# Performance work log

Measured on AMD Instinct MI355X. Metric: run time of the kernel, lower is better.

Reference implementation:

```python
import jax, jax.numpy as jnp
import numpy as np

B, H, W, C = 2, 96, 96, 96
GROUPS = 32
EPS = 1e-5


def group_norm_dim1(x, gamma, beta):
    # Faithful to torch nn.GroupNorm(32, C) applied to an NHWC tensor:
    # dim 1 (H) is treated as the channel axis, normalized over (H//G, W, C) per group.
    b, h, w, c = x.shape
    xg = x.reshape(b, GROUPS, h // GROUPS, w, c)
    mean = xg.mean(axis=(2, 3, 4), keepdims=True)
    var = xg.var(axis=(2, 3, 4), keepdims=True)
    xn = ((xg - mean) * jax.lax.rsqrt(var + EPS)).reshape(b, h, w, c)
    return xn * gamma[None, :, None, None] + beta[None, :, None, None]


def setup_inputs() -> dict:
    key = jax.random.key(0)
    ks = jax.random.split(key, 9)
    s = 1.0 / np.sqrt(C)  # kaiming-uniform-ish scale
    x = jax.random.normal(ks[0], (B, H, W, C), dtype=jnp.float32)
    Wq = jax.random.uniform(ks[1], (C, C), jnp.float32, -s, s)
    Wk = jax.random.uniform(ks[2], (C, C), jnp.float32, -s, s)
    Wv = jax.random.uniform(ks[3], (C, C), jnp.float32, -s, s)
    Wp = jax.random.uniform(ks[4], (C, C), jnp.float32, -s, s)
    return {
        "x": x,
        "gamma": jnp.ones((H,), jnp.float32),   # GroupNorm affine weight (over dim 1)
        "beta": jnp.zeros((H,), jnp.float32),
        "Wq": Wq, "bq": jnp.zeros((C,), jnp.float32),
        "Wk": Wk, "bk": jnp.zeros((C,), jnp.float32),
        "Wv": Wv, "bv": jnp.zeros((C,), jnp.float32),
        "Wp": Wp, "bp": jnp.zeros((C,), jnp.float32),
    }


def reference(x, gamma, beta, Wq, bq, Wk, bk, Wv, bv, Wp, bp):
    b, h, w, c = x.shape
    hn = group_norm_dim1(x, gamma, beta)
    q = hn @ Wq + bq  # [B,H,W,C], Nin = contract last dim
    k = hn @ Wk + bk
    v = hn @ Wv + bv
    scale = c ** (-0.5)
    # full dense spatial attention: [B, HW, HW]
    scores = jnp.einsum('bxyc,buvc->bxyuv', q, k) * scale
    attn = jax.nn.softmax(scores.reshape(b, h, w, h * w), axis=-1).reshape(b, h, w, h, w)
    o = jnp.einsum('bxyuv,buvc->bxyc', attn, v)
    return x + (o @ Wp + bp)
```

## Files before the change

kernel.cpp:

```cpp
#include <hip/hip_runtime.h>
#include <hip/hip_bf16.h>
#include <stdint.h>

#define B_   2
#define H_   96
#define W_   96
#define C_   96
#define HW_  (H_ * W_)
#define NT_  (B_ * HW_)
#define EPS_ 1e-5f
#define KSPLIT  8
#define KRANGE  (HW_ / KSPLIT)
#define ATT_NIT (KRANGE / 32)
#define SCL (0.10206207261596575f * 1.4426950408889634f)

typedef __hip_bfloat16 bf16;
typedef __attribute__((ext_vector_type(8))) short short8;
typedef __attribute__((ext_vector_type(16))) float f32x16;

__device__ __forceinline__ uint32_t pk_bf16(float a, float b) {
    uint32_t ua = __float_as_uint(a) + 0x8000u;
    uint32_t ub = __float_as_uint(b) + 0x8000u;
    return __builtin_amdgcn_perm(ub, ua, 0x07060302u);
}
__device__ __forceinline__ float bl(uint32_t u) { uint32_t x = u << 16;         return *(float*)&x; }
__device__ __forceinline__ float bh(uint32_t u) { uint32_t x = u & 0xffff0000u; return *(float*)&x; }
__device__ __forceinline__ float fexp2(float x) { return __builtin_amdgcn_exp2f(x); }
__device__ __forceinline__ short8 lds_frag(const short* p) {
    union { int2 h[2]; short8 v; } t;
    t.h[0] = *(const int2*)(p);
    t.h[1] = *(const int2*)(p + 4);
    return t.v;
}

__device__ __forceinline__ void load_hn_frags(
        const float* __restrict__ x, const float2* __restrict__ stats,
        const float* __restrict__ gamma, const float* __restrict__ beta,
        int token, int hh, short8* hf) {
    int b = token / HW_;
    int h = (token % HW_) / W_;
    float2 st = stats[b * 32 + h / 3];
    float g0 = gamma[h];
    float ga = g0 * st.y;
    float be = beta[h] - st.x * st.y * g0;
    const float* xr = x + (size_t)token * C_ + hh * 8;
    #pragma unroll
    for (int s = 0; s < 6; ++s) {
        float4 a = *(const float4*)(xr + s * 16);
        float4 c = *(const float4*)(xr + s * 16 + 4);
        union { uint32_t w[4]; short8 v; } f;
        f.w[0] = pk_bf16(a.x * ga + be, a.y * ga + be);
        f.w[1] = pk_bf16(a.z * ga + be, a.w * ga + be);
        f.w[2] = pk_bf16(c.x * ga + be, c.y * ga + be);
        f.w[3] = pk_bf16(c.z * ga + be, c.w * ga + be);
        hf[s] = f.v;
    }
}

__global__ __launch_bounds__(1024)
void stats_prep_kernel(const float* __restrict__ x, float2* __restrict__ stats,
                       const float* __restrict__ Wq, const float* __restrict__ Wk,
                       const float* __restrict__ Wv, const float* __restrict__ Wp,
                       bf16* __restrict__ wqt, bf16* __restrict__ wkt,
                       bf16* __restrict__ wvt, bf16* __restrict__ wpt) {
    int blk = blockIdx.x;
    int tid = threadIdx.x;
    if (blk >= 64) {
        int wsel = blk - 64;
        const float* S = (wsel == 0) ? Wq : (wsel == 1) ? Wk : (wsel == 2) ? Wv : Wp;
        bf16* D = (wsel == 0) ? wqt : (wsel == 1) ? wkt : (wsel == 2) ? wvt : wpt;
        for (int i = tid; i < C_ * C_; i += 1024) {
            int r = i / C_, c = i % C_;
            D[c * C_ + r] = __float2bfloat16(S[r * C_ + c]);
        }
        return;
    }
    int b = blk >> 5, g = blk & 31;
    const int n4 = 3 * W_ * C_ / 4;
    const float4* xb = (const float4*)(x + (size_t)(b * H_ + 3 * g) * (W_ * C_));
    float s = 0.f, ss = 0.f;
    for (int i = tid; i < n4; i += 1024) {
        float4 v = xb[i];
        s  += v.x + v.y + v.z + v.w;
        ss += v.x * v.x + v.y * v.y + v.z * v.z + v.w * v.w;
    }
    #pragma unroll
    for (int off = 1; off < 64; off <<= 1) {
        s  += __shfl_xor(s, off, 64);
        ss += __shfl_xor(ss, off, 64);
    }
    __shared__ float rs[16], rss[16];
    int wid = tid >> 6;
    if ((tid & 63) == 0) { rs[wid] = s; rss[wid] = ss; }
    __syncthreads();
    if (tid == 0) {
        float ts = 0.f, tss = 0.f;
        #pragma unroll
        for (int i = 0; i < 16; ++i) { ts += rs[i]; tss += rss[i]; }
        const float n = 3 * W_ * C_;
        float mean = ts / n;
        float var  = tss / n - mean * mean;
        stats[blk] = make_float2(mean, rsqrtf(var + EPS_));
    }
}

__global__ __launch_bounds__(64)
void qkv_kernel(const float* __restrict__ x, const float2* __restrict__ stats,
                const float* __restrict__ gamma, const float* __restrict__ beta,
                const bf16* __restrict__ wqt, const bf16* __restrict__ wkt,
                const bf16* __restrict__ wvt,
                const float* __restrict__ bq, const float* __restrict__ bk,
                const float* __restrict__ bv,
                bf16* __restrict__ qb, bf16* __restrict__ kb, bf16* __restrict__ vt) {
    int blk = blockIdx.x;
    int w = blk / 576, tile = blk % 576;
    int n0 = tile * 32;
    int lane = threadIdx.x;
    int col = lane & 31, hh = lane >> 5;
    int token = n0 + col;

    short8 hf[6];
    load_hn_frags(x, stats, gamma, beta, token, hh, hf);

    if (w == 2) {
        int bb = n0 / HW_, nl0 = n0 % HW_;
        #pragma unroll
        for (int t = 0; t < 3; ++t) {
            int c = t * 32 + col;
            const bf16* wrow = wvt + (size_t)c * C_ + hh * 8;
            f32x16 acc = (f32x16)(0.f);
            #pragma unroll
            for (int s = 0; s < 6; ++s)
                acc = __builtin_amdgcn_mfma_f32_32x32x16_bf16(
                        hf[s], *(const short8*)(wrow + s * 16), acc, 0, 0, 0);
            float bias = bv[c];
            bf16* dst = vt + ((size_t)bb * C_ + c) * HW_ + nl0 + 4 * hh;
            #pragma unroll
            for (int g = 0; g < 4; ++g) {
                uint2 pk = make_uint2(pk_bf16(acc[4 * g] + bias, acc[4 * g + 1] + bias),
                                      pk_bf16(acc[4 * g + 2] + bias, acc[4 * g + 3] + bias));
                *(uint2*)(dst + 8 * g) = pk;
            }
        }
    } else {
        const bf16*  wt   = (w == 0) ? wqt : wkt;
        const float* bias = (w == 0) ? bq : bk;
        bf16*        dst  = (w == 0) ? qb : kb;
        float        scl  = (w == 0) ? SCL : 1.f;
        #pragma unroll
        for (int t = 0; t < 3; ++t) {
            const bf16* wrow = wt + (size_t)(t * 32 + col) * C_ + hh * 8;
            f32x16 acc = (f32x16)(0.f);
            #pragma unroll
            for (int s = 0; s < 6; ++s)
                acc = __builtin_amdgcn_mfma_f32_32x32x16_bf16(
                        *(const short8*)(wrow + s * 16), hf[s], acc, 0, 0, 0);
            #pragma unroll
            for (int g = 0; g < 4; ++g) {
                int nb = t * 32 + 8 * g + 4 * hh;
                float4 b4 = *(const float4*)(bias + nb);
                float v0 = (acc[4 * g]     + b4.x) * scl;
                float v1 = (acc[4 * g + 1] + b4.y) * scl;
                float v2 = (acc[4 * g + 2] + b4.z) * scl;
                float v3 = (acc[4 * g + 3] + b4.w) * scl;
                uint2 pk = make_uint2(pk_bf16(v0, v1), pk_bf16(v2, v3));
                *(uint2*)(dst + (size_t)token * C_ + nb) = pk;
            }
        }
    }
}

__global__ __launch_bounds__(256, 4)
void attn_kernel(const bf16* __restrict__ qb, const bf16* __restrict__ kb,
                 const bf16* __restrict__ vt,
                 bf16* __restrict__ pob, float* __restrict__ pl) {
    __shared__ short Kbuf[2][32 * 100];
    __shared__ short Vbuf[2][96 * 36];

    int blk = blockIdx.x;
    int ks = blk & 7, qg = blk >> 3;
    int b = qg / 72, g72 = qg % 72;
    int n0 = g72 * 128;
    int tid = threadIdx.x;
    int wave = tid >> 6, lane = tid & 63;
    int col = lane & 31, hh = lane >> 5;

    const bf16* kbb = kb + ((size_t)b * HW_ + (size_t)ks * KRANGE) * C_;
    const bf16* vbb = vt + (size_t)b * C_ * HW_ + (size_t)ks * KRANGE;

    int n = n0 + wave * 32 + col;
    short8 qf[6];
    {
        const bf16* qrow = qb + (size_t)(b * HW_ + n) * C_ + hh * 8;
        #pragma unroll
        for (int s = 0; s < 6; ++s) qf[s] = *(const short8*)(qrow + s * 16);
    }

    f32x16 oa[3];
    #pragma unroll
    for (int t = 0; t < 3; ++t) oa[t] = (f32x16)(0.f);
    float l_run = 0.f;

    bool isK = (tid < 128);
    int t128 = tid & 127;
    int ldsA[3], ldsB[3], goff[3];
    #pragma unroll
    for (int j = 0; j < 3; ++j) {
        int c = t128 + 128 * j;
        if (isK) {
            ldsA[j] = (c / 12) * 100 + (c % 12) * 8;
            ldsB[j] = ldsA[j] + 4;
            goff[j] = c * 8;
        } else {
            int rw = c >> 2, g = c & 3;
            ldsA[j] = rw * 36 + (2 * g - (g & 1)) * 4;
            ldsB[j] = rw * 36 + (2 * g + 2 - (g & 1)) * 4;
            goff[j] = rw * HW_ + g * 8;
        }
    }
    const bf16* gbase = isK ? kbb : vbb;
    const int itstep = isK ? (32 * C_) : 32;

    {
        short* sb = isK ? Kbuf[0] : Vbuf[0];
        #pragma unroll
        for (int j = 0; j < 3; ++j) {
            int4 r = *(const int4*)(gbase + goff[j]);
            *(int2*)(sb + ldsA[j]) = make_int2(r.x, r.y);
            *(int2*)(sb + ldsB[j]) = make_int2(r.z, r.w);
        }
    }
    __syncthreads();

    union FU { uint32_t w[4]; short8 v; };

    for (int it = 0; it < ATT_NIT; ++it) {
        int cur = it & 1;
        bool pre = (it + 1 < ATT_NIT);
        int4 r0, r1, r2;
        if (pre) {
            const bf16* g = gbase + (size_t)(it + 1) * itstep;
            r0 = *(const int4*)(g + goff[0]);
            r1 = *(const int4*)(g + goff[1]);
            r2 = *(const int4*)(g + goff[2]);
        }

        const short* Kc = Kbuf[cur];
        const short* Vc = Vbuf[cur];

        short8 kf[6];
        #pragma unroll
        for (int s = 0; s < 6; ++s)
            kf[s] = lds_frag(Kc + col * 100 + s * 16 + hh * 8);

        f32x16 st = (f32x16)(0.f);
        #pragma unroll
        for (int s = 0; s < 6; ++s)
            st = __builtin_amdgcn_mfma_f32_32x32x16_bf16(kf[s], qf[s], st, 0, 0, 0);

        float p[16], ls = 0.f;
        #pragma unroll
        for (int i = 0; i < 16; ++i) { p[i] = fexp2(st[i]); ls += p[i]; }
        l_run += ls;
        FU f0, f1;
        #pragma unroll
        for (int j = 0; j < 4; ++j) {
            f0.w[j] = pk_bf16(p[2 * j],     p[2 * j + 1]);
            f1.w[j] = pk_bf16(p[8 + 2 * j], p[8 + 2 * j + 1]);
        }

        #pragma unroll
        for (int t = 0; t < 3; ++t) {
            const short* vr = Vc + (32 * t + col) * 36 + hh * 8;
            short8 vf0 = lds_frag(vr);
            short8 vf1 = lds_frag(vr + 16);
            oa[t] = __builtin_amdgcn_mfma_f32_32x32x16_bf16(vf0, f0.v, oa[t], 0, 0, 0);
            oa[t] = __builtin_amdgcn_mfma_f32_32x32x16_bf16(vf1, f1.v, oa[t], 0, 0, 0);
        }

        if (pre) {
            short* sb = isK ? Kbuf[cur ^ 1] : Vbuf[cur ^ 1];
            *(int2*)(sb + ldsA[0]) = make_int2(r0.x, r0.y);
            *(int2*)(sb + ldsB[0]) = make_int2(r0.z, r0.w);
            *(int2*)(sb + ldsA[1]) = make_int2(r1.x, r1.y);
            *(int2*)(sb + ldsB[1]) = make_int2(r1.z, r1.w);
            *(int2*)(sb + ldsA[2]) = make_int2(r2.x, r2.y);
            *(int2*)(sb + ldsB[2]) = make_int2(r2.z, r2.w);
        }
        __syncthreads();
    }

    {
        size_t bq = (size_t)b * HW_ + n;
        float lt = l_run + __shfl_xor(l_run, 32, 64);
        if (hh == 0) pl[(size_t)ks * NT_ + bq] = lt;
        #pragma unroll
        for (int t = 0; t < 3; ++t)
            #pragma unroll
            for (int g = 0; g < 4; ++g) {
                int c0 = t * 32 + 8 * g + 4 * hh;
                uint2 pk = make_uint2(
                    pk_bf16(oa[t][4 * g],     oa[t][4 * g + 1]),
                    pk_bf16(oa[t][4 * g + 2], oa[t][4 * g + 3]));
                *(uint2*)(pob + ((size_t)ks * NT_ + bq) * C_ + c0) = pk;
            }
    }
}

__global__ __launch_bounds__(256)
void out_kernel(const float* __restrict__ x,
                const bf16* __restrict__ pob, const float* __restrict__ pl,
                const bf16* __restrict__ wpt, const float* __restrict__ bp,
                float* __restrict__ out) {
    __shared__ short ofs[32 * 100];
    __shared__ float linv_s[32];

    int tile = blockIdx.x;
    int n0 = tile * 32;
    int tid = threadIdx.x;

    if (tid < 32) {
        int token = n0 + tid;
        float l = 0.f;
        #pragma unroll
        for (int ksp = 0; ksp < KSPLIT; ++ksp) l += pl[(size_t)ksp * NT_ + token];
        linv_s[tid] = 1.f / l;
    }
    __syncthreads();

    for (int pos = tid; pos < 384; pos += 256) {
        int token = pos / 12, c8 = (pos % 12) * 8;
        float acc[8] = {0.f, 0.f, 0.f, 0.f, 0.f, 0.f, 0.f, 0.f};
        #pragma unroll
        for (int ksp = 0; ksp < KSPLIT; ++ksp) {
            uint4 u = *(const uint4*)(pob + ((size_t)ksp * NT_ + n0 + token) * C_ + c8);
            acc[0] += bl(u.x); acc[1] += bh(u.x);
            acc[2] += bl(u.y); acc[3] += bh(u.y);
            acc[4] += bl(u.z); acc[5] += bh(u.z);
            acc[6] += bl(u.w); acc[7] += bh(u.w);
        }
        float inv = linv_s[token];
        short* dst = ofs + token * 100 + c8;
        *(int2*)(dst)     = make_int2(pk_bf16(acc[0] * inv, acc[1] * inv),
                                      pk_bf16(acc[2] * inv, acc[3] * inv));
        *(int2*)(dst + 4) = make_int2(pk_bf16(acc[4] * inv, acc[5] * inv),
                                      pk_bf16(acc[6] * inv, acc[7] * inv));
    }
    __syncthreads();

    int wave = tid >> 6;
    if (wave >= 3) return;
    int lane = tid & 63, col = lane & 31, hh = lane >> 5;
    int t = wave;
    int token = n0 + col;

    short8 of[6];
    #pragma unroll
    for (int s = 0; s < 6; ++s)
        of[s] = lds_frag(ofs + col * 100 + s * 16 + hh * 8);

    f32x16 acc = (f32x16)(0.f);
    const bf16* wrow = wpt + (size_t)(t * 32 + col) * C_ + hh * 8;
    #pragma unroll
    for (int s = 0; s < 6; ++s)
        acc = __builtin_amdgcn_mfma_f32_32x32x16_bf16(
                *(const short8*)(wrow + s * 16), of[s], acc, 0, 0, 0);
    #pragma unroll
    for (int g = 0; g < 4; ++g) {
        int nb = t * 32 + 8 * g + 4 * hh;
        float4 b4 = *(const float4*)(bp + nb);
        float4 xv = *(const float4*)(x + (size_t)token * C_ + nb);
        float4 rr;
        rr.x = xv.x + acc[4 * g]     + b4.x;
        rr.y = xv.y + acc[4 * g + 1] + b4.y;
        rr.z = xv.z + acc[4 * g + 2] + b4.z;
        rr.w = xv.w + acc[4 * g + 3] + b4.w;
        *(float4*)(out + (size_t)token * C_ + nb) = rr;
    }
}

extern "C" void kernel_launch(void* const* d_in, const int* in_sizes, int n_in,
                              void* d_out, int out_size, void* d_ws, size_t ws_size,
                              hipStream_t stream) {
    const float* x     = (const float*)d_in[0];
    const float* gamma = (const float*)d_in[1];
    const float* beta  = (const float*)d_in[2];
    const float* Wq    = (const float*)d_in[3];
    const float* bq    = (const float*)d_in[4];
    const float* Wk    = (const float*)d_in[5];
    const float* bk    = (const float*)d_in[6];
    const float* Wv    = (const float*)d_in[7];
    const float* bv    = (const float*)d_in[8];
    const float* Wp    = (const float*)d_in[9];
    const float* bp    = (const float*)d_in[10];
    float* out = (float*)d_out;

    char* ws = (char*)d_ws;
    const size_t TB = (size_t)NT_ * C_ * 2;
    bf16* qb  = (bf16*)(ws);
    bf16* kb  = (bf16*)(ws + TB);
    bf16* vt  = (bf16*)(ws + 2 * TB);
    bf16* wqt = (bf16*)(ws + 3 * TB);
    bf16* wkt = (bf16*)(ws + 3 * TB + 18432);
    bf16* wvt = (bf16*)(ws + 3 * TB + 2 * 18432);
    bf16* wpt = (bf16*)(ws + 3 * TB + 3 * 18432);
    float2* stats = (float2*)(ws + 3 * TB + 4 * 18432);
    bf16*  pob = (bf16*)(ws + 3 * TB + 4 * 18432 + 512);
    float* pl  = (float*)(ws + 3 * TB + 4 * 18432 + 512
                          + (size_t)KSPLIT * NT_ * C_ * 2);

    hipLaunchKernelGGL(stats_prep_kernel, dim3(68), dim3(1024), 0, stream,
                       x, stats, Wq, Wk, Wv, Wp, wqt, wkt, wvt, wpt);
    hipLaunchKernelGGL(qkv_kernel, dim3(3 * 576), dim3(64), 0, stream,
                       x, stats, gamma, beta, wqt, wkt, wvt, bq, bk, bv, qb, kb, vt);
    hipLaunchKernelGGL(attn_kernel, dim3(1152), dim3(256), 0, stream,
                       qb, kb, vt, pob, pl);
    hipLaunchKernelGGL(out_kernel, dim3(576), dim3(256), 0, stream,
                       x, pob, pl, wpt, bp, out);
}
```

Before: 195.8 us.

## Triple-buffer K/V tiles and software-pipeline QK^T one iteration ahead

```diff
diff --git a/kernel.cpp b/kernel.cpp
--- a/kernel.cpp
+++ b/kernel.cpp
@@ -170,12 +170,12 @@
     }
 }
 
-__global__ __launch_bounds__(256, 4)
+__global__ __launch_bounds__(256, 3)
 void attn_kernel(const bf16* __restrict__ qb, const bf16* __restrict__ kb,
                  const bf16* __restrict__ vt,
                  bf16* __restrict__ pob, float* __restrict__ pl) {
-    __shared__ short Kbuf[2][32 * 100];
-    __shared__ short Vbuf[2][96 * 36];
+    __shared__ short Kbuf[3][32 * 100];
+    __shared__ short Vbuf[3][96 * 36];
 
     int blk = blockIdx.x;
     int ks = blk & 7, qg = blk >> 3;
@@ -222,73 +222,112 @@
     const int itstep = isK ? (32 * C_) : 32;
 
     {
-        short* sb = isK ? Kbuf[0] : Vbuf[0];
+        short* sb0 = isK ? Kbuf[0] : Vbuf[0];
+        short* sb1 = isK ? Kbuf[1] : Vbuf[1];
         #pragma unroll
         for (int j = 0; j < 3; ++j) {
             int4 r = *(const int4*)(gbase + goff[j]);
-            *(int2*)(sb + ldsA[j]) = make_int2(r.x, r.y);
-            *(int2*)(sb + ldsB[j]) = make_int2(r.z, r.w);
+            *(int2*)(sb0 + ldsA[j]) = make_int2(r.x, r.y);
+            *(int2*)(sb0 + ldsB[j]) = make_int2(r.z, r.w);
+        }
+        #pragma unroll
+        for (int j = 0; j < 3; ++j) {
+            int4 r = *(const int4*)(gbase + itstep + goff[j]);
+            *(int2*)(sb1 + ldsA[j]) = make_int2(r.x, r.y);
+            *(int2*)(sb1 + ldsB[j]) = make_int2(r.z, r.w);
         }
     }
     __syncthreads();
 
     union FU { uint32_t w[4]; short8 v; };
 
-    for (int it = 0; it < ATT_NIT; ++it) {
-        int cur = it & 1;
-        bool pre = (it + 1 < ATT_NIT);
-        int4 r0, r1, r2;
-        if (pre) {
-            const bf16* g = gbase + (size_t)(it + 1) * itstep;
-            r0 = *(const int4*)(g + goff[0]);
-            r1 = *(const int4*)(g + goff[1]);
-            r2 = *(const int4*)(g + goff[2]);
-        }
-
-        const short* Kc = Kbuf[cur];
-        const short* Vc = Vbuf[cur];
-
+    f32x16 stA, stB;
+    {
+        const short* Kc = Kbuf[0];
         short8 kf[6];
         #pragma unroll
         for (int s = 0; s < 6; ++s)
             kf[s] = lds_frag(Kc + col * 100 + s * 16 + hh * 8);
-
-        f32x16 st = (f32x16)(0.f);
+        stA = (f32x16)(0.f);
         #pragma unroll
         for (int s = 0; s < 6; ++s)
-            st = __builtin_amdgcn_mfma_f32_32x32x16_bf16(kf[s], qf[s], st, 0, 0, 0);
-
-        float p[16], ls = 0.f;
-        #pragma unroll
-        for (int i = 0; i < 16; ++i) { p[i] = fexp2(st[i]); ls += p[i]; }
-        l_run += ls;
-        FU f0, f1;
-        #pragma unroll
-        for (int j = 0; j < 4; ++j) {
-            f0.w[j] = pk_bf16(p[2 * j],     p[2 * j + 1]);
-            f1.w[j] = pk_bf16(p[8 + 2 * j], p[8 + 2 * j + 1]);
-        }
-
-        #pragma unroll
-        for (int t = 0; t < 3; ++t) {
-            const short* vr = Vc + (32 * t + col) * 36 + hh * 8;
-            short8 vf0 = lds_frag(vr);
-            short8 vf1 = lds_frag(vr + 16);
-            oa[t] = __builtin_amdgcn_mfma_f32_32x32x16_bf16(vf0, f0.v, oa[t], 0, 0, 0);
-            oa[t] = __builtin_amdgcn_mfma_f32_32x32x16_bf16(vf1, f1.v, oa[t], 0, 0, 0);
-        }
-
-        if (pre) {
-            short* sb = isK ? Kbuf[cur ^ 1] : Vbuf[cur ^ 1];
-            *(int2*)(sb + ldsA[0]) = make_int2(r0.x, r0.y);
-            *(int2*)(sb + ldsB[0]) = make_int2(r0.z, r0.w);
-            *(int2*)(sb + ldsA[1]) = make_int2(r1.x, r1.y);
-            *(int2*)(sb + ldsB[1]) = make_int2(r1.z, r1.w);
-            *(int2*)(sb + ldsA[2]) = make_int2(r2.x, r2.y);
-            *(int2*)(sb + ldsB[2]) = make_int2(r2.z, r2.w);
-        }
-        __syncthreads();
-    }
+            stA = __builtin_amdgcn_mfma_f32_32x32x16_bf16(kf[s], qf[s], stA, 0, 0, 0);
+    }
+
+#define ATT_BODY(IT, CUR, NXT, WRT, SC, SN, PRE1, PRE2)                          \
+    {                                                                            \
+        int4 r0, r1, r2;                                                         \
+        if (PRE2) {                                                              \
+            const bf16* g = gbase + (size_t)((IT) + 2) * itstep;                 \
+            r0 = *(const int4*)(g + goff[0]);                                    \
+            r1 = *(const int4*)(g + goff[1]);                                    \
+            r2 = *(const int4*)(g + goff[2]);                                    \
+        }                                                                        \
+        if (PRE1) {                                                              \
+            const short* Kc = Kbuf[NXT];                                         \
+            short8 kf0 = lds_frag(Kc + col * 100 + 0 * 16 + hh * 8);             \
+            short8 kf1 = lds_frag(Kc + col * 100 + 1 * 16 + hh * 8);             \
+            short8 kf2 = lds_frag(Kc + col * 100 + 2 * 16 + hh * 8);             \
+            short8 kf3 = lds_frag(Kc + col * 100 + 3 * 16 + hh * 8);             \
+            short8 kf4 = lds_frag(Kc + col * 100 + 4 * 16 + hh * 8);             \
+            short8 kf5 = lds_frag(Kc + col * 100 + 5 * 16 + hh * 8);             \
+            SN = (f32x16)(0.f);                                                  \
+            SN = __builtin_amdgcn_mfma_f32_32x32x16_bf16(kf0, qf[0], SN, 0, 0, 0); \
+            SN = __builtin_amdgcn_mfma_f32_32x32x16_bf16(kf1, qf[1], SN, 0, 0, 0); \
+            SN = __builtin_amdgcn_mfma_f32_32x32x16_bf16(kf2, qf[2], SN, 0, 0, 0); \
+            SN = __builtin_amdgcn_mfma_f32_32x32x16_bf16(kf3, qf[3], SN, 0, 0, 0); \
+            SN = __builtin_amdgcn_mfma_f32_32x32x16_bf16(kf4, qf[4], SN, 0, 0, 0); \
+            SN = __builtin_amdgcn_mfma_f32_32x32x16_bf16(kf5, qf[5], SN, 0, 0, 0); \
+        }                                                                        \
+        float p[16], ls = 0.f;                                                   \
+        _Pragma("unroll")                                                        \
+        for (int i = 0; i < 16; ++i) { p[i] = fexp2(SC[i]); ls += p[i]; }        \
+        l_run += ls;                                                             \
+        FU f0, f1;                                                               \
+        _Pragma("unroll")                                                        \
+        for (int j = 0; j < 4; ++j) {                                            \
+            f0.w[j] = pk_bf16(p[2 * j],     p[2 * j + 1]);                       \
+            f1.w[j] = pk_bf16(p[8 + 2 * j], p[8 + 2 * j + 1]);                   \
+        }                                                                        \
+        {                                                                        \
+            const short* Vc = Vbuf[CUR];                                         \
+            _Pragma("unroll")                                                    \
+            for (int t = 0; t < 3; ++t) {                                        \
+                const short* vr = Vc + (32 * t + col) * 36 + hh * 8;             \
+                short8 vf0 = lds_frag(vr);                                       \
+                short8 vf1 = lds_frag(vr + 16);                                  \
+                oa[t] = __builtin_amdgcn_mfma_f32_32x32x16_bf16(vf0, f0.v, oa[t], 0, 0, 0); \
+                oa[t] = __builtin_amdgcn_mfma_f32_32x32x16_bf16(vf1, f1.v, oa[t], 0, 0, 0); \
+            }                                                                    \
+        }                                                                        \
+        if (PRE2) {                                                              \
+            short* sb = isK ? Kbuf[WRT] : Vbuf[WRT];                             \
+            *(int2*)(sb + ldsA[0]) = make_int2(r0.x, r0.y);                      \
+            *(int2*)(sb + ldsB[0]) = make_int2(r0.z, r0.w);                      \
+            *(int2*)(sb + ldsA[1]) = make_int2(r1.x, r1.y);                      \
+            *(int2*)(sb + ldsB[1]) = make_int2(r1.z, r1.w);                      \
+            *(int2*)(sb + ldsA[2]) = make_int2(r2.x, r2.y);                      \
+            *(int2*)(sb + ldsB[2]) = make_int2(r2.z, r2.w);                      \
+        }                                                                        \
+        __syncthreads();                                                         \
+    }
+
+    #pragma unroll 1
+    for (int itb = 0; itb < ATT_NIT - 6; itb += 6) {
+        ATT_BODY(itb + 0, 0, 1, 2, stA, stB, 1, 1)
+        ATT_BODY(itb + 1, 1, 2, 0, stB, stA, 1, 1)
+        ATT_BODY(itb + 2, 2, 0, 1, stA, stB, 1, 1)
+        ATT_BODY(itb + 3, 0, 1, 2, stB, stA, 1, 1)
+        ATT_BODY(itb + 4, 1, 2, 0, stA, stB, 1, 1)
+        ATT_BODY(itb + 5, 2, 0, 1, stB, stA, 1, 1)
+    }
+    ATT_BODY(30, 0, 1, 2, stA, stB, 1, 1)
+    ATT_BODY(31, 1, 2, 0, stB, stA, 1, 1)
+    ATT_BODY(32, 2, 0, 1, stA, stB, 1, 1)
+    ATT_BODY(33, 0, 1, 2, stB, stA, 1, 1)
+    ATT_BODY(34, 1, 2, 0, stA, stB, 1, 0)
+    ATT_BODY(35, 2, 0, 1, stB, stA, 0, 0)
+#undef ATT_BODY
 
     {
         size_t bq = (size_t)b * HW_ + n;
```

New measurement: 304.1 us. 1.55x slower.

## Software-pipeline attention loop: overlap PV MMA of previous tile with softmax

Applied to the files above, without the earlier changes.

```diff
diff --git a/kernel.cpp b/kernel.cpp
--- a/kernel.cpp
+++ b/kernel.cpp
@@ -17,6 +17,8 @@
 typedef __hip_bfloat16 bf16;
 typedef __attribute__((ext_vector_type(8))) short short8;
 typedef __attribute__((ext_vector_type(16))) float f32x16;
+
+union FU { uint32_t w[4]; short8 v; };
 
 __device__ __forceinline__ uint32_t pk_bf16(float a, float b) {
     uint32_t ua = __float_as_uint(a) + 0x8000u;
@@ -170,12 +172,83 @@
     }
 }
 
-__global__ __launch_bounds__(256, 4)
+template<int KB, int VPV, int VWR, bool DO_PV, bool PRE>
+__device__ __forceinline__ void att_body(
+        int it,
+        short (&Kbuf)[2][3200], short (&Vbuf)[3][3456],
+        const short8 (&qf)[6], f32x16 (&oa)[3],
+        FU& f0, FU& f1, float& l_run,
+        const bf16* gbase, int goff0, int goff1, int goff2,
+        int ldsA0, int ldsA1, int ldsA2,
+        int ldsB0, int ldsB1, int ldsB2,
+        int itstep, bool isK, int col, int hh) {
+    int4 r0, r1, r2;
+    if (PRE) {
+        const bf16* g = gbase + (size_t)(it + 1) * itstep;
+        r0 = *(const int4*)(g + goff0);
+        r1 = *(const int4*)(g + goff1);
+        r2 = *(const int4*)(g + goff2);
+    }
+    FU p0, p1;
+    p0.v = f0.v; p1.v = f1.v;
+
+    __builtin_amdgcn_s_setprio(1);
+    const short* Kc = Kbuf[KB];
+    short8 kf0 = lds_frag(Kc + col * 100 + 0 * 16 + hh * 8);
+    short8 kf1 = lds_frag(Kc + col * 100 + 1 * 16 + hh * 8);
+    short8 kf2 = lds_frag(Kc + col * 100 + 2 * 16 + hh * 8);
+    short8 kf3 = lds_frag(Kc + col * 100 + 3 * 16 + hh * 8);
+    short8 kf4 = lds_frag(Kc + col * 100 + 4 * 16 + hh * 8);
+    short8 kf5 = lds_frag(Kc + col * 100 + 5 * 16 + hh * 8);
+    f32x16 st = (f32x16)(0.f);
+    st = __builtin_amdgcn_mfma_f32_32x32x16_bf16(kf0, qf[0], st, 0, 0, 0);
+    st = __builtin_amdgcn_mfma_f32_32x32x16_bf16(kf1, qf[1], st, 0, 0, 0);
+    st = __builtin_amdgcn_mfma_f32_32x32x16_bf16(kf2, qf[2], st, 0, 0, 0);
+    st = __builtin_amdgcn_mfma_f32_32x32x16_bf16(kf3, qf[3], st, 0, 0, 0);
+    st = __builtin_amdgcn_mfma_f32_32x32x16_bf16(kf4, qf[4], st, 0, 0, 0);
+    st = __builtin_amdgcn_mfma_f32_32x32x16_bf16(kf5, qf[5], st, 0, 0, 0);
+
+    if (DO_PV) {
+        const short* Vc = Vbuf[VPV];
+        #pragma unroll
+        for (int t = 0; t < 3; ++t) {
+            const short* vr = Vc + (32 * t + col) * 36 + hh * 8;
+            short8 vf0 = lds_frag(vr);
+            short8 vf1 = lds_frag(vr + 16);
+            oa[t] = __builtin_amdgcn_mfma_f32_32x32x16_bf16(vf0, p0.v, oa[t], 0, 0, 0);
+            oa[t] = __builtin_amdgcn_mfma_f32_32x32x16_bf16(vf1, p1.v, oa[t], 0, 0, 0);
+        }
+    }
+
+    float p[16], ls = 0.f;
+    #pragma unroll
+    for (int i = 0; i < 16; ++i) { p[i] = fexp2(st[i]); ls += p[i]; }
+    l_run += ls;
+    #pragma unroll
+    for (int j = 0; j < 4; ++j) {
+        f0.w[j] = pk_bf16(p[2 * j],     p[2 * j + 1]);
+        f1.w[j] = pk_bf16(p[8 + 2 * j], p[8 + 2 * j + 1]);
+    }
+    __builtin_amdgcn_s_setprio(0);
+
+    if (PRE) {
+        short* sb = isK ? (short*)Kbuf[KB ^ 1] : (short*)Vbuf[VWR];
+        *(int2*)(sb + ldsA0) = make_int2(r0.x, r0.y);
+        *(int2*)(sb + ldsB0) = make_int2(r0.z, r0.w);
+        *(int2*)(sb + ldsA1) = make_int2(r1.x, r1.y);
+        *(int2*)(sb + ldsB1) = make_int2(r1.z, r1.w);
+        *(int2*)(sb + ldsA2) = make_int2(r2.x, r2.y);
+        *(int2*)(sb + ldsB2) = make_int2(r2.z, r2.w);
+    }
+    __syncthreads();
+}
+
+__global__ __launch_bounds__(256, 2)
 void attn_kernel(const bf16* __restrict__ qb, const bf16* __restrict__ kb,
                  const bf16* __restrict__ vt,
                  bf16* __restrict__ pob, float* __restrict__ pl) {
     __shared__ short Kbuf[2][32 * 100];
-    __shared__ short Vbuf[2][96 * 36];
+    __shared__ short Vbuf[3][96 * 36];
 
     int blk = blockIdx.x;
     int ks = blk & 7, qg = blk >> 3;
@@ -222,7 +295,7 @@
     const int itstep = isK ? (32 * C_) : 32;
 
     {
-        short* sb = isK ? Kbuf[0] : Vbuf[0];
+        short* sb = isK ? (short*)Kbuf[0] : (short*)Vbuf[0];
         #pragma unroll
         for (int j = 0; j < 3; ++j) {
             int4 r = *(const int4*)(gbase + goff[j]);
@@ -232,43 +305,34 @@
     }
     __syncthreads();
 
-    union FU { uint32_t w[4]; short8 v; };
-
-    for (int it = 0; it < ATT_NIT; ++it) {
-        int cur = it & 1;
-        bool pre = (it + 1 < ATT_NIT);
-        int4 r0, r1, r2;
-        if (pre) {
-            const bf16* g = gbase + (size_t)(it + 1) * itstep;
-            r0 = *(const int4*)(g + goff[0]);
-            r1 = *(const int4*)(g + goff[1]);
-            r2 = *(const int4*)(g + goff[2]);
-        }
-
-        const short* Kc = Kbuf[cur];
-        const short* Vc = Vbuf[cur];
-
-        short8 kf[6];
-        #pragma unroll
-        for (int s = 0; s < 6; ++s)
-            kf[s] = lds_frag(Kc + col * 100 + s * 16 + hh * 8);
-
-        f32x16 st = (f32x16)(0.f);
-        #pragma unroll
-        for (int s = 0; s < 6; ++s)
-            st = __builtin_amdgcn_mfma_f32_32x32x16_bf16(kf[s], qf[s], st, 0, 0, 0);
-
-        float p[16], ls = 0.f;
-        #pragma unroll
-        for (int i = 0; i < 16; ++i) { p[i] = fexp2(st[i]); ls += p[i]; }
-        l_run += ls;
-        FU f0, f1;
-        #pragma unroll
-        for (int j = 0; j < 4; ++j) {
-            f0.w[j] = pk_bf16(p[2 * j],     p[2 * j + 1]);
-            f1.w[j] = pk_bf16(p[8 + 2 * j], p[8 + 2 * j + 1]);
-        }
-
+    FU f0, f1;
+    f0.v = (short8)(short)0; f1.v = (short8)(short)0;
+
+    #define ABODY(KB_, VPV_, VWR_, DOPV_, PRE_, IT_)                         \
+        att_body<KB_, VPV_, VWR_, DOPV_, PRE_>(IT_, Kbuf, Vbuf, qf, oa,      \
+            f0, f1, l_run, gbase, goff[0], goff[1], goff[2],                 \
+            ldsA[0], ldsA[1], ldsA[2], ldsB[0], ldsB[1], ldsB[2],            \
+            itstep, isK, col, hh)
+
+    ABODY(0, 0, 1, 0, 1, 0);
+    #pragma unroll 1
+    for (int ib = 1; ib <= 25; ib += 6) {
+        ABODY(1, 0, 2, 1, 1, ib + 0);
+        ABODY(0, 1, 0, 1, 1, ib + 1);
+        ABODY(1, 2, 1, 1, 1, ib + 2);
+        ABODY(0, 0, 2, 1, 1, ib + 3);
+        ABODY(1, 1, 0, 1, 1, ib + 4);
+        ABODY(0, 2, 1, 1, 1, ib + 5);
+    }
+    ABODY(1, 0, 2, 1, 1, 31);
+    ABODY(0, 1, 0, 1, 1, 32);
+    ABODY(1, 2, 1, 1, 1, 33);
+    ABODY(0, 0, 2, 1, 1, 34);
+    ABODY(1, 1, 0, 1, 0, 35);
+    #undef ABODY
+
+    {
+        const short* Vc = Vbuf[2];
         #pragma unroll
         for (int t = 0; t < 3; ++t) {
             const short* vr = Vc + (32 * t + col) * 36 + hh * 8;
@@ -277,17 +341,6 @@
             oa[t] = __builtin_amdgcn_mfma_f32_32x32x16_bf16(vf0, f0.v, oa[t], 0, 0, 0);
             oa[t] = __builtin_amdgcn_mfma_f32_32x32x16_bf16(vf1, f1.v, oa[t], 0, 0, 0);
         }
-
-        if (pre) {
-            short* sb = isK ? Kbuf[cur ^ 1] : Vbuf[cur ^ 1];
-            *(int2*)(sb + ldsA[0]) = make_int2(r0.x, r0.y);
-            *(int2*)(sb + ldsB[0]) = make_int2(r0.z, r0.w);
-            *(int2*)(sb + ldsA[1]) = make_int2(r1.x, r1.y);
-            *(int2*)(sb + ldsB[1]) = make_int2(r1.z, r1.w);
-            *(int2*)(sb + ldsA[2]) = make_int2(r2.x, r2.y);
-            *(int2*)(sb + ldsB[2]) = make_int2(r2.z, r2.w);
-        }
-        __syncthreads();
     }
 
     {
```

After: 199.9 us. 1.02x slower.

## Process two query tiles per wave in attention to reuse K/V fragments

Applied to the files above, without the earlier changes.

```diff
diff --git a/kernel.cpp b/kernel.cpp
--- a/kernel.cpp
+++ b/kernel.cpp
@@ -170,7 +170,7 @@
     }
 }
 
-__global__ __launch_bounds__(256, 4)
+__global__ __launch_bounds__(256, 2)
 void attn_kernel(const bf16* __restrict__ qb, const bf16* __restrict__ kb,
                  const bf16* __restrict__ vt,
                  bf16* __restrict__ pob, float* __restrict__ pl) {
@@ -179,8 +179,8 @@
 
     int blk = blockIdx.x;
     int ks = blk & 7, qg = blk >> 3;
-    int b = qg / 72, g72 = qg % 72;
-    int n0 = g72 * 128;
+    int b = qg / 36, g36 = qg % 36;
+    int n0 = g36 * 256;
     int tid = threadIdx.x;
     int wave = tid >> 6, lane = tid & 63;
     int col = lane & 31, hh = lane >> 5;
@@ -188,18 +188,22 @@
     const bf16* kbb = kb + ((size_t)b * HW_ + (size_t)ks * KRANGE) * C_;
     const bf16* vbb = vt + (size_t)b * C_ * HW_ + (size_t)ks * KRANGE;
 
-    int n = n0 + wave * 32 + col;
-    short8 qf[6];
+    int nA = n0 + wave * 32 + col;
+    int nB = nA + 128;
+    short8 qfA[6], qfB[6];
     {
-        const bf16* qrow = qb + (size_t)(b * HW_ + n) * C_ + hh * 8;
-        #pragma unroll
-        for (int s = 0; s < 6; ++s) qf[s] = *(const short8*)(qrow + s * 16);
-    }
-
-    f32x16 oa[3];
-    #pragma unroll
-    for (int t = 0; t < 3; ++t) oa[t] = (f32x16)(0.f);
-    float l_run = 0.f;
+        const bf16* qrowA = qb + (size_t)(b * HW_ + nA) * C_ + hh * 8;
+        const bf16* qrowB = qb + (size_t)(b * HW_ + nB) * C_ + hh * 8;
+        #pragma unroll
+        for (int s = 0; s < 6; ++s) qfA[s] = *(const short8*)(qrowA + s * 16);
+        #pragma unroll
+        for (int s = 0; s < 6; ++s) qfB[s] = *(const short8*)(qrowB + s * 16);
+    }
+
+    f32x16 oaA[3], oaB[3];
+    #pragma unroll
+    for (int t = 0; t < 3; ++t) { oaA[t] = (f32x16)(0.f); oaB[t] = (f32x16)(0.f); }
+    float lA = 0.f, lB = 0.f;
 
     bool isK = (tid < 128);
     int t128 = tid & 127;
@@ -253,20 +257,37 @@
         for (int s = 0; s < 6; ++s)
             kf[s] = lds_frag(Kc + col * 100 + s * 16 + hh * 8);
 
-        f32x16 st = (f32x16)(0.f);
+        f32x16 stA = (f32x16)(0.f);
         #pragma unroll
         for (int s = 0; s < 6; ++s)
-            st = __builtin_amdgcn_mfma_f32_32x32x16_bf16(kf[s], qf[s], st, 0, 0, 0);
-
-        float p[16], ls = 0.f;
-        #pragma unroll
-        for (int i = 0; i < 16; ++i) { p[i] = fexp2(st[i]); ls += p[i]; }
-        l_run += ls;
-        FU f0, f1;
-        #pragma unroll
-        for (int j = 0; j < 4; ++j) {
-            f0.w[j] = pk_bf16(p[2 * j],     p[2 * j + 1]);
-            f1.w[j] = pk_bf16(p[8 + 2 * j], p[8 + 2 * j + 1]);
+            stA = __builtin_amdgcn_mfma_f32_32x32x16_bf16(kf[s], qfA[s], stA, 0, 0, 0);
+        f32x16 stB = (f32x16)(0.f);
+        #pragma unroll
+        for (int s = 0; s < 6; ++s)
+            stB = __builtin_amdgcn_mfma_f32_32x32x16_bf16(kf[s], qfB[s], stB, 0, 0, 0);
+
+        FU f0A, f1A, f0B, f1B;
+        {
+            float p[16], ls = 0.f;
+            #pragma unroll
+            for (int i = 0; i < 16; ++i) { p[i] = fexp2(stA[i]); ls += p[i]; }
+            lA += ls;
+            #pragma unroll
+            for (int j = 0; j < 4; ++j) {
+                f0A.w[j] = pk_bf16(p[2 * j],     p[2 * j + 1]);
+                f1A.w[j] = pk_bf16(p[8 + 2 * j], p[8 + 2 * j + 1]);
+            }
+        }
+        {
+            float p[16], ls = 0.f;
+            #pragma unroll
+            for (int i = 0; i < 16; ++i) { p[i] = fexp2(stB[i]); ls += p[i]; }
+            lB += ls;
+            #pragma unroll
+            for (int j = 0; j < 4; ++j) {
+                f0B.w[j] = pk_bf16(p[2 * j],     p[2 * j + 1]);
+                f1B.w[j] = pk_bf16(p[8 + 2 * j], p[8 + 2 * j + 1]);
+            }
         }
 
         #pragma unroll
@@ -274,8 +295,10 @@
             const short* vr = Vc + (32 * t + col) * 36 + hh * 8;
             short8 vf0 = lds_frag(vr);
             short8 vf1 = lds_frag(vr + 16);
-            oa[t] = __builtin_amdgcn_mfma_f32_32x32x16_bf16(vf0, f0.v, oa[t], 0, 0, 0);
-            oa[t] = __builtin_amdgcn_mfma_f32_32x32x16_bf16(vf1, f1.v, oa[t], 0, 0, 0);
+            oaA[t] = __builtin_amdgcn_mfma_f32_32x32x16_bf16(vf0, f0A.v, oaA[t], 0, 0, 0);
+            oaA[t] = __builtin_amdgcn_mfma_f32_32x32x16_bf16(vf1, f1A.v, oaA[t], 0, 0, 0);
+            oaB[t] = __builtin_amdgcn_mfma_f32_32x32x16_bf16(vf0, f0B.v, oaB[t], 0, 0, 0);
+            oaB[t] = __builtin_amdgcn_mfma_f32_32x32x16_bf16(vf1, f1B.v, oaB[t], 0, 0, 0);
         }
 
         if (pre) {
@@ -291,18 +314,27 @@
     }
 
     {
-        size_t bq = (size_t)b * HW_ + n;
-        float lt = l_run + __shfl_xor(l_run, 32, 64);
-        if (hh == 0) pl[(size_t)ks * NT_ + bq] = lt;
+        size_t bqA = (size_t)b * HW_ + nA;
+        size_t bqB = (size_t)b * HW_ + nB;
+        float ltA = lA + __shfl_xor(lA, 32, 64);
+        float ltB = lB + __shfl_xor(lB, 32, 64);
+        if (hh == 0) {
+            pl[(size_t)ks * NT_ + bqA] = ltA;
+            pl[(size_t)ks * NT_ + bqB] = ltB;
+        }
         #pragma unroll
         for (int t = 0; t < 3; ++t)
             #pragma unroll
             for (int g = 0; g < 4; ++g) {
                 int c0 = t * 32 + 8 * g + 4 * hh;
-                uint2 pk = make_uint2(
-                    pk_bf16(oa[t][4 * g],     oa[t][4 * g + 1]),
-                    pk_bf16(oa[t][4 * g + 2], oa[t][4 * g + 3]));
-                *(uint2*)(pob + ((size_t)ks * NT_ + bq) * C_ + c0) = pk;
+                uint2 pkA = make_uint2(
+                    pk_bf16(oaA[t][4 * g],     oaA[t][4 * g + 1]),
+                    pk_bf16(oaA[t][4 * g + 2], oaA[t][4 * g + 3]));
+                *(uint2*)(pob + ((size_t)ks * NT_ + bqA) * C_ + c0) = pkA;
+                uint2 pkB = make_uint2(
+                    pk_bf16(oaB[t][4 * g],     oaB[t][4 * g + 1]),
+                    pk_bf16(oaB[t][4 * g + 2], oaB[t][4 * g + 3]));
+                *(uint2*)(pob + ((size_t)ks * NT_ + bqB) * C_ + c0) = pkB;
             }
     }
 }
@@ -413,7 +445,7 @@
                        x, stats, Wq, Wk, Wv, Wp, wqt, wkt, wvt, wpt);
     hipLaunchKernelGGL(qkv_kernel, dim3(3 * 576), dim3(64), 0, stream,
                        x, stats, gamma, beta, wqt, wkt, wvt, bq, bk, bv, qb, kb, vt);
-    hipLaunchKernelGGL(attn_kernel, dim3(1152), dim3(256), 0, stream,
+    hipLaunchKernelGGL(attn_kernel, dim3(576), dim3(256), 0, stream,
                        qb, kb, vt, pob, pl);
     hipLaunchKernelGGL(out_kernel, dim3(576), dim3(256), 0, stream,
                        x, pob, pl, wpt, bp, out);
```

After: 194.3 us. About the same (-0.8%).
